# Performance work log

Measured on AMD Instinct MI355X. Metric: run time of the kernel, lower is better.

## Reference

```python
import jax, jax.numpy as jnp
import numpy as np

N_BUILDING = 30
N_SEMANTIC = 11
D_MODEL = 256
B_GRAPHS = 2048
EDGES_PER_GRAPH = 240
N_NODES = B_GRAPHS * N_BUILDING
N_EDGES = B_GRAPHS * EDGES_PER_GRAPH


def setup_inputs() -> dict:
    key = jax.random.key(0)
    ks = jax.random.split(key, 24)
    geometry = jax.random.normal(ks[0], (N_NODES, 5), dtype=jnp.float32)
    semantic = jax.random.randint(ks[1], (N_NODES,), 0, N_SEMANTIC)
    # within-graph edges
    src_l = jax.random.randint(ks[2], (N_EDGES,), 0, N_BUILDING)
    dst_l = jax.random.randint(ks[3], (N_EDGES,), 0, N_BUILDING)
    off = jnp.repeat(jnp.arange(B_GRAPHS) * N_BUILDING, EDGES_PER_GRAPH)
    edge_index = jnp.stack([src_l + off, dst_l + off])
    batch = jnp.repeat(jnp.arange(B_GRAPHS), N_BUILDING)

    def lin(k, i, o):
        k1, k2 = jax.random.split(k)
        s = 1.0 / np.sqrt(i)
        return (jax.random.uniform(k1, (i, o), jnp.float32, -s, s),
                jax.random.uniform(k2, (o,), jnp.float32, -s, s))

    W_geo, b_geo = lin(ks[4], 5, D_MODEL)
    emb = jax.random.normal(ks[5], (N_SEMANTIC, D_MODEL), dtype=jnp.float32)
    W_lot, b_lot = lin(ks[6], 2 * D_MODEL + N_BUILDING, D_MODEL)
    W_mp1, b_mp1 = lin(ks[7], 2 * D_MODEL, D_MODEL)
    W_mp2, b_mp2 = lin(ks[8], 2 * D_MODEL, D_MODEL)
    W_mp3, b_mp3 = lin(ks[9], 2 * D_MODEL, D_MODEL)
    W_agg, b_agg = lin(ks[10], 4 * D_MODEL, D_MODEL)
    W_mu, b_mu = lin(ks[11], D_MODEL, D_MODEL)
    W_var, b_var = lin(ks[12], D_MODEL, D_MODEL)
    return dict(geometry=geometry, semantic=semantic, edge_index=edge_index, batch=batch,
                W_geo=W_geo, b_geo=b_geo, emb=emb, W_lot=W_lot, b_lot=b_lot,
                W_mp1=W_mp1, b_mp1=b_mp1, W_mp2=W_mp2, b_mp2=b_mp2,
                W_mp3=W_mp3, b_mp3=b_mp3, W_agg=W_agg, b_agg=b_agg,
                W_mu=W_mu, b_mu=b_mu, W_var=W_var, b_var=b_var)


def _msgpass(x, src, dst, W, b):
    # PyG: x_i = x[dst] (target), x_j = x[src]; message = Linear(cat[x_i, x_j]); mean-aggregate at dst
    msgs = jnp.concatenate([x[dst], x[src]], axis=1) @ W + b  # [E, D]
    n = x.shape[0]
    s = jax.ops.segment_sum(msgs, dst, num_segments=n)
    cnt = jax.ops.segment_sum(jnp.ones((msgs.shape[0], 1), msgs.dtype), dst, num_segments=n)
    return s / jnp.maximum(cnt, 1.0)


def reference(geometry, semantic, edge_index, batch,
              W_geo, b_geo, emb, W_lot, b_lot,
              W_mp1, b_mp1, W_mp2, b_mp2, W_mp3, b_mp3,
              W_agg, b_agg, W_mu, b_mu, W_var, b_var):
    n_graphs = geometry.shape[0] // N_BUILDING
    src, dst = edge_index[0], edge_index[1]
    enc_geo = geometry @ W_geo + b_geo                       # [N, D]
    enc_sem = emb[semantic]                                   # [N, D]
    x_pos = jnp.tile(jnp.eye(N_BUILDING, dtype=jnp.float32), (n_graphs, 1))  # [N, 30]
    h = jnp.concatenate([enc_geo, enc_sem, x_pos], axis=1)
    h = jax.nn.relu(h @ W_lot + b_lot)
    g0 = jax.ops.segment_max(h, batch, num_segments=n_graphs)
    h = jax.nn.relu(_msgpass(h, src, dst, W_mp1, b_mp1))
    g1 = jax.ops.segment_max(h, batch, num_segments=n_graphs)
    h = jax.nn.relu(_msgpass(h, src, dst, W_mp2, b_mp2))
    g2 = jax.ops.segment_max(h, batch, num_segments=n_graphs)
    h = jax.nn.relu(_msgpass(h, src, dst, W_mp3, b_mp3))
    g3 = jax.ops.segment_max(h, batch, num_segments=n_graphs)
    g = jnp.concatenate([g0, g1, g2, g3], axis=1)             # [B, 4D]
    latent = g @ W_agg + b_agg
    mu = latent @ W_mu + b_mu
    log_var = latent @ W_var + b_var
    return mu, log_var
```

## Files before the change

kernel.cpp:

```cpp
#include <hip/hip_runtime.h>

typedef unsigned short u16;
typedef unsigned int u32;
typedef __attribute__((ext_vector_type(8))) short bf8;
typedef __attribute__((ext_vector_type(4))) float f4;
typedef __attribute__((ext_vector_type(4))) int i4;

#define NB  30
#define BG  2048
#define EPG 240
#define NEg (BG*EPG)
#define SA  260
#define SS  40
#define SL  264
#define SG  1032

#define WOFF_WT    0
#define WOFF_WAGG  786432
#define WOFF_WMU   (786432+524288)
#define WOFF_WVAR  (786432+524288+131072)
#define WOFF_TAB   (786432+524288+262144)
#define WOFF_G     (WOFF_TAB + 48128)
#define WOFF_FLAG  (WOFF_G + 4194304)

__device__ __forceinline__ float us2f(u16 u) {
    union { u32 i; float f; } v; v.i = ((u32)u) << 16; return v.f;
}
__device__ __forceinline__ u16 f2us(float f) {
    union { float f; u32 u; } v; v.f = f;
    u32 u = v.u;
    return (u16)((u + 0x7FFFu + ((u >> 16) & 1u)) >> 16);
}
__device__ __forceinline__ int ldidx(const void* p, long long i, int i64) {
    return i64 ? (int)((const long long*)p)[i] : ((const int*)p)[i];
}

__global__ __launch_bounds__(256) void prep_kernel(
    const float* __restrict__ Wmp1, const float* __restrict__ Wmp2,
    const float* __restrict__ Wmp3, const float* __restrict__ Wagg,
    const float* __restrict__ Wmu,  const float* __restrict__ Wvar,
    const float* __restrict__ W_geo, const float* __restrict__ b_geo,
    const float* __restrict__ emb,   const float* __restrict__ W_lot,
    const float* __restrict__ b_lot,
    const void* __restrict__ edge,  const void* __restrict__ semA,
    char* __restrict__ ws, int* __restrict__ flags)
{
    const int t = threadIdx.x;
    const int b = blockIdx.x;

    if (b == 209) {
        if (t == 0) {
            const int* e32 = (const int*)edge;
            int zc = 0;
            for (int j = 1; j <= 31; j += 2) if (e32[j] == 0) zc++;
            flags[0] = (zc == 16) ? 1 : 0;
            flags[1] = 0;
        }
        return;
    }

    if (b >= 192) {
        float* tab = (float*)(ws + WOFF_TAB);
        const int d = t, b2 = b - 192;
        if (b2 < 5) {
            float a = 0.f;
            #pragma unroll 8
            for (int k = 0; k < 256; ++k)
                a = fmaf(W_geo[b2*256 + k], W_lot[k*256 + d], a);
            tab[b2*256 + d] = a;
        } else if (b2 < 16) {
            const int s = b2 - 5;
            float a = 0.f;
            #pragma unroll 8
            for (int k = 0; k < 256; ++k)
                a = fmaf(emb[s*256 + k], W_lot[(256 + k)*256 + d], a);
            tab[1536 + s*256 + d] = a;
        } else {
            float a = b_lot[d];
            #pragma unroll 8
            for (int k = 0; k < 256; ++k)
                a = fmaf(b_geo[k], W_lot[k*256 + d], a);
            tab[1280 + d] = a;
            for (int p = 0; p < NB; ++p)
                tab[4352 + p*256 + d] = W_lot[(512 + p)*256 + d];
        }
        return;
    }

    __shared__ short tile[64 * 65];
    const float* W; u16* Wt; int K32, bk, bn;
    if (b < 96)       { const int r = b/32, tt = b%32;
                        W = (r==0)?Wmp1:((r==1)?Wmp2:Wmp3);
                        Wt = (u16*)(ws + WOFF_WT) + (size_t)r*256*512;
                        K32 = 16;  bk = tt/4;  bn = tt%4; }
    else if (b < 160) { const int tt = b-96;
                        W = Wagg; Wt = (u16*)(ws + WOFF_WAGG);
                        K32 = 32; bk = tt/4;  bn = tt%4; }
    else if (b < 176) { const int tt = b-160;
                        W = Wmu;  Wt = (u16*)(ws + WOFF_WMU);
                        K32 = 8;  bk = tt/4;  bn = tt%4; }
    else              { const int tt = b-176;
                        W = Wvar; Wt = (u16*)(ws + WOFF_WVAR);
                        K32 = 8;  bk = tt/4;  bn = tt%4; }

    const int r = t >> 6, c = t & 63;
    const int k0 = bk*64, n0 = bn*64;
    #pragma unroll
    for (int i = 0; i < 16; ++i) {
        const int kk = r + i*4;
        tile[kk*65 + c] = (short)f2us(W[(size_t)(k0 + kk)*256 + n0 + c]);
    }
    __syncthreads();

    const int lane = t >> 2;
    const int j0   = (t & 3) * 2;
    const int quad = lane >> 4, l16 = lane & 15;
    #pragma unroll
    for (int dk = 0; dk < 2; ++dk) {
        const int ktf = bk*2 + dk;
        #pragma unroll
        for (int nt = 0; nt < 4; ++nt) {
            const int chunk = (bn*K32 + ktf)*4 + nt;
            u32* dst = (u32*)(Wt + (size_t)chunk*512);
            const int kl = dk*32 + quad*8 + j0;
            const int nl = nt*16 + l16;
            const u32 v = (u32)(u16)tile[kl*65 + nl] |
                          ((u32)(u16)tile[(kl+1)*65 + nl] << 16);
            dst[t] = v;
        }
    }
}

__global__ __launch_bounds__(256, 4) void graph_kernel(
    const float* __restrict__ geometry,
    const void* __restrict__ semantic,
    const void* __restrict__ edge_index,
    const float* __restrict__ bmp1, const float* __restrict__ bmp2,
    const float* __restrict__ bmp3,
    const char* __restrict__ ws, u16* __restrict__ G,
    const int* __restrict__ flags)
{
    __shared__ __align__(16) short Ahi[32*SA];
    __shared__ __align__(16) short Shi[32*SS];
    __shared__ __align__(16) short Slo[32*SS];
    __shared__ int   cntN[32];
    __shared__ float geo_l[NB*5];
    __shared__ int   sem_l[NB];

    int* cntC = (int*)Ahi;

    const int tid  = threadIdx.x;
    const int g    = blockIdx.x;
    const int wave = tid >> 6, lane = tid & 63;
    const int l16  = lane & 15, quad = lane >> 4;

    const int i64 = flags[0];
    const u16* WtAll = (const u16*)(ws + WOFF_WT);
    const float* tab = (const float*)(ws + WOFF_TAB);

    {
        i4 z = {0, 0, 0, 0};
        ((i4*)cntC)[tid] = z;
        if (tid < 65) ((i4*)&Ahi[30*SA])[tid] = z;
        if (tid < 160) { ((i4*)Shi)[tid] = z; ((i4*)Slo)[tid] = z; }
        if (tid < 32) cntN[tid] = 0;
        if (tid < NB*5) geo_l[tid] = geometry[(size_t)g*NB*5 + tid];
        if (tid < NB)   sem_l[tid] = ldidx(semantic, g*NB + tid, i64);
    }
    __syncthreads();

    if (tid < EPG) {
        const long long e = (long long)g*EPG + tid;
        const int s  = ldidx(edge_index, e,                  i64) - g*NB;
        const int dd = ldidx(edge_index, (long long)NEg + e, i64) - g*NB;
        atomicAdd(&cntC[dd*32 + s], 1);
        atomicAdd(&cntN[dd], 1);
    }
    __syncthreads();

    for (int i = tid; i < 960; i += 256) {
        const int n = i >> 5, m = i & 31;
        const int c = cntC[n*32 + m], cn = cntN[n];
        const float v = (cn > 0) ? (float)c / (float)cn : 0.f;
        const u16 hi = f2us(v);
        Shi[n*SS + m] = (short)hi;
        Slo[n*SS + m] = (short)f2us(v - us2f(hi));
    }
    __syncthreads();

    {
        const int d = tid;
        const float m0 = tab[0*256+d], m1 = tab[1*256+d], m2 = tab[2*256+d],
                    m3 = tab[3*256+d], m4 = tab[4*256+d];
        const float cD = tab[1280 + d];
        float gmax = 0.f;
        for (int n = 0; n < NB; ++n) {
            const int s = sem_l[n];
            float a = cD + tab[1536 + s*256 + d] + tab[4352 + n*256 + d];
            a = fmaf(geo_l[n*5+0], m0, a); a = fmaf(geo_l[n*5+1], m1, a);
            a = fmaf(geo_l[n*5+2], m2, a); a = fmaf(geo_l[n*5+3], m3, a);
            a = fmaf(geo_l[n*5+4], m4, a);
            const float v = fmaxf(a, 0.f);
            Ahi[n*SA + d] = (short)f2us(v);
            gmax = fmaxf(gmax, v);
        }
        G[(size_t)g*1024 + d] = f2us(gmax);
    }
    __syncthreads();

    unsigned rmask = 0;
    #pragma unroll
    for (int mt = 0; mt < 2; ++mt)
        #pragma unroll
        for (int i = 0; i < 4; ++i) {
            const int row = mt*16 + quad*4 + i;
            if (row < NB && cntN[row] > 0) rmask |= 1u << (mt*4 + i);
        }

    bf8 sh[2], sl[2];
    #pragma unroll
    for (int mo = 0; mo < 2; ++mo) {
        sh[mo] = *(const bf8*)&Shi[(mo*16 + l16)*SS + quad*8];
        sl[mo] = *(const bf8*)&Slo[(mo*16 + l16)*SS + quad*8];
    }
    const int srcbase = ((quad & 1) << 5) | l16;
    const int mtsel   = quad >> 1;

    for (int r = 0; r < 3; ++r) {
        const u16* Wsw = WtAll + (size_t)r*131072;

        f4 C1[2][4], P[2][4];
        #pragma unroll
        for (int mt = 0; mt < 2; ++mt)
            #pragma unroll
            for (int nt = 0; nt < 4; ++nt) {
                C1[mt][nt] = (f4){0.f, 0.f, 0.f, 0.f};
                P [mt][nt] = (f4){0.f, 0.f, 0.f, 0.f};
            }

        #pragma unroll
        for (int kt = 0; kt < 8; ++kt) {
            bf8 ah[2];
            #pragma unroll
            for (int mt = 0; mt < 2; ++mt)
                ah[mt] = *(const bf8*)&Ahi[(mt*16 + l16)*SA + kt*32 + quad*8];
            #pragma unroll
            for (int nt = 0; nt < 4; ++nt) {
                const bf8 bt = *(const bf8*)&Wsw[(size_t)(((wave*16 + kt  )*4 + nt))*512 + lane*8];
                const bf8 bb = *(const bf8*)&Wsw[(size_t)(((wave*16 + kt+8)*4 + nt))*512 + lane*8];
                #pragma unroll
                for (int mt = 0; mt < 2; ++mt) {
                    C1[mt][nt] = __builtin_amdgcn_mfma_f32_16x16x32_bf16(ah[mt], bt, C1[mt][nt], 0, 0, 0);
                    P [mt][nt] = __builtin_amdgcn_mfma_f32_16x16x32_bf16(ah[mt], bb, P [mt][nt], 0, 0, 0);
                }
            }
        }

        unsigned pk[2][4][2];
        #pragma unroll
        for (int mt = 0; mt < 2; ++mt)
            #pragma unroll
            for (int nt = 0; nt < 4; ++nt) {
                pk[mt][nt][0] = (u32)f2us(P[mt][nt][0]) | ((u32)f2us(P[mt][nt][1]) << 16);
                pk[mt][nt][1] = (u32)f2us(P[mt][nt][2]) | ((u32)f2us(P[mt][nt][3]) << 16);
            }

        #pragma unroll
        for (int nt = 0; nt < 4; ++nt) {
            union { bf8 v; u32 u[4]; } bf_;
            #pragma unroll
            for (int t2 = 0; t2 < 4; ++t2) {
                const int src = srcbase + ((t2 >> 1) << 4);
                const u32 v0 = __shfl(pk[0][nt][t2 & 1], src, 64);
                const u32 v1 = __shfl(pk[1][nt][t2 & 1], src, 64);
                bf_.u[t2] = mtsel ? v1 : v0;
            }
            #pragma unroll
            for (int mo = 0; mo < 2; ++mo) {
                C1[mo][nt] = __builtin_amdgcn_mfma_f32_16x16x32_bf16(sh[mo], bf_.v, C1[mo][nt], 0, 0, 0);
                C1[mo][nt] = __builtin_amdgcn_mfma_f32_16x16x32_bf16(sl[mo], bf_.v, C1[mo][nt], 0, 0, 0);
            }
        }
        __syncthreads();

        const float* br = (r == 0) ? bmp1 : ((r == 1) ? bmp2 : bmp3);
        #pragma unroll
        for (int nt = 0; nt < 4; ++nt) {
            const int col = wave*64 + nt*16 + l16;
            const float bias = br[col];
            float cmax = 0.f;
            #pragma unroll
            for (int mt = 0; mt < 2; ++mt)
                #pragma unroll
                for (int i = 0; i < 4; ++i) {
                    const int row = mt*16 + quad*4 + i;
                    float v = fmaxf(C1[mt][nt][i] + bias, 0.f);
                    if (!((rmask >> (mt*4 + i)) & 1u)) v = 0.f;
                    Ahi[row*SA + col] = (short)f2us(v);
                    cmax = fmaxf(cmax, v);
                }
            cmax = fmaxf(cmax, __shfl_xor(cmax, 16, 64));
            cmax = fmaxf(cmax, __shfl_xor(cmax, 32, 64));
            if (quad == 0)
                G[(size_t)g*1024 + (r+1)*256 + col] = f2us(cmax);
        }
        __syncthreads();
    }
}

__global__ __launch_bounds__(256, 4) void head_kernel(
    const char* __restrict__ ws, const u16* __restrict__ G,
    const float* __restrict__ bagg, const float* __restrict__ bmu,
    const float* __restrict__ bvar, float* __restrict__ out)
{
    __shared__ __align__(16) short Gs[8*SG];
    __shared__ __align__(16) short Lhi[16*SL];
    __shared__ __align__(16) short Llo[16*SL];

    const int tid  = threadIdx.x;
    const int wave = tid >> 6, lane = tid & 63;
    const int l16  = lane & 15, quad = lane >> 4;
    const int g0   = blockIdx.x * 8;

    const u16* WtA = (const u16*)(ws + WOFF_WAGG);
    const u16* WtM = (const u16*)(ws + WOFF_WMU);
    const u16* WtV = (const u16*)(ws + WOFF_WVAR);

    #pragma unroll
    for (int rr = 0; rr < 8; ++rr) {
        ((u32*)&Gs[rr*SG])[tid]       = ((const u32*)&G[(size_t)(g0+rr)*1024])[tid];
        ((u32*)&Gs[rr*SG])[tid + 256] = ((const u32*)&G[(size_t)(g0+rr)*1024])[tid + 256];
    }
    __syncthreads();

    f4 acc[4];
    #pragma unroll
    for (int nt = 0; nt < 4; ++nt) acc[nt] = (f4){0.f, 0.f, 0.f, 0.f};

    #pragma unroll 8
    for (int kt = 0; kt < 32; ++kt) {
        const bf8 ah = *(const bf8*)&Gs[(l16 & 7)*SG + kt*32 + quad*8];
        #pragma unroll
        for (int nt = 0; nt < 4; ++nt) {
            const bf8 b = *(const bf8*)&WtA[(size_t)((wave*32 + kt)*4 + nt)*512 + lane*8];
            acc[nt] = __builtin_amdgcn_mfma_f32_16x16x32_bf16(ah, b, acc[nt], 0, 0, 0);
        }
    }
    #pragma unroll
    for (int nt = 0; nt < 4; ++nt) {
        const int col = wave*64 + nt*16 + l16;
        const float bias = bagg[col];
        #pragma unroll
        for (int i = 0; i < 4; ++i) {
            const int row = quad*4 + i;
            const float v = acc[nt][i] + bias;
            const u16 hi = f2us(v);
            Lhi[row*SL + col] = (short)hi;
            Llo[row*SL + col] = (short)f2us(v - us2f(hi));
        }
    }
    __syncthreads();

    f4 am[4], av[4];
    #pragma unroll
    for (int nt = 0; nt < 4; ++nt) {
        am[nt] = (f4){0.f, 0.f, 0.f, 0.f};
        av[nt] = (f4){0.f, 0.f, 0.f, 0.f};
    }
    #pragma unroll
    for (int kt = 0; kt < 8; ++kt) {
        const bf8 ah = *(const bf8*)&Lhi[l16*SL + kt*32 + quad*8];
        const bf8 al = *(const bf8*)&Llo[l16*SL + kt*32 + quad*8];
        #pragma unroll
        for (int nt = 0; nt < 4; ++nt) {
            const bf8 bm_ = *(const bf8*)&WtM[(size_t)((wave*8 + kt)*4 + nt)*512 + lane*8];
            const bf8 bv_ = *(const bf8*)&WtV[(size_t)((wave*8 + kt)*4 + nt)*512 + lane*8];
            am[nt] = __builtin_amdgcn_mfma_f32_16x16x32_bf16(ah, bm_, am[nt], 0, 0, 0);
            am[nt] = __builtin_amdgcn_mfma_f32_16x16x32_bf16(al, bm_, am[nt], 0, 0, 0);
            av[nt] = __builtin_amdgcn_mfma_f32_16x16x32_bf16(ah, bv_, av[nt], 0, 0, 0);
            av[nt] = __builtin_amdgcn_mfma_f32_16x16x32_bf16(al, bv_, av[nt], 0, 0, 0);
        }
    }
    #pragma unroll
    for (int nt = 0; nt < 4; ++nt) {
        const int col = wave*64 + nt*16 + l16;
        const float b1 = bmu[col], b2 = bvar[col];
        #pragma unroll
        for (int i = 0; i < 4; ++i) {
            const int r = quad*4 + i;
            if (r < 8) {
                const int row = g0 + r;
                out[(size_t)row*256 + col]          = am[nt][i] + b1;
                out[524288 + (size_t)row*256 + col] = av[nt][i] + b2;
            }
        }
    }
}

extern "C" void kernel_launch(void* const* d_in, const int* in_sizes, int n_in,
                              void* d_out, int out_size, void* d_ws, size_t ws_size,
                              hipStream_t stream)
{
    const float* geometry  = (const float*)d_in[0];
    const void*  semantic  = d_in[1];
    const void*  edge_ix   = d_in[2];
    const float* W_geo = (const float*)d_in[4];
    const float* b_geo = (const float*)d_in[5];
    const float* emb   = (const float*)d_in[6];
    const float* W_lot = (const float*)d_in[7];
    const float* b_lot = (const float*)d_in[8];
    const float* Wmp1  = (const float*)d_in[9];
    const float* bmp1  = (const float*)d_in[10];
    const float* Wmp2  = (const float*)d_in[11];
    const float* bmp2  = (const float*)d_in[12];
    const float* Wmp3  = (const float*)d_in[13];
    const float* bmp3  = (const float*)d_in[14];
    const float* Wagg  = (const float*)d_in[15];
    const float* bagg  = (const float*)d_in[16];
    const float* Wmu   = (const float*)d_in[17];
    const float* bmu   = (const float*)d_in[18];
    const float* Wvar  = (const float*)d_in[19];
    const float* bvar  = (const float*)d_in[20];

    char* ws    = (char*)d_ws;
    int*  flags = (int*)(ws + WOFF_FLAG);
    u16*  G     = (u16*)(ws + WOFF_G);

    prep_kernel<<<210, 256, 0, stream>>>(Wmp1, Wmp2, Wmp3, Wagg, Wmu, Wvar,
                                         W_geo, b_geo, emb, W_lot, b_lot,
                                         edge_ix, semantic, ws, flags);
    graph_kernel<<<BG, 256, 0, stream>>>(geometry, semantic, edge_ix,
                                         bmp1, bmp2, bmp3, ws, G, flags);
    head_kernel<<<256, 256, 0, stream>>>(ws, G, bagg, bmu, bvar, (float*)d_out);
}
```

Measured before the change: 237.2 us.

## Process two graphs per block in graph_kernel to reuse weight fragments

Each block of graph_kernel now handles two graphs, holding two sets of LDS buffers and accumulators, so every weight fragment loaded from global memory feeds MFMAs for both graphs. The aim is to halve the weight traffic per graph in the three message-passing rounds. In exchange the block doubles its LDS use and accumulator registers, launch bounds drop from 4 to 3 waves per SIMD, and only 1024 blocks are launched, which may reduce occupancy and latency hiding.

After: 341.0 us. 43.8% more time.

```diff
diff --git a/kernel.cpp b/kernel.cpp
--- a/kernel.cpp
+++ b/kernel.cpp
@@ -131,7 +131,7 @@
     }
 }
 
-__global__ __launch_bounds__(256, 4) void graph_kernel(
+__global__ __launch_bounds__(256, 3) void graph_kernel(
     const float* __restrict__ geometry,
     const void* __restrict__ semantic,
     const void* __restrict__ edge_index,
@@ -140,17 +140,15 @@
     const char* __restrict__ ws, u16* __restrict__ G,
     const int* __restrict__ flags)
 {
-    __shared__ __align__(16) short Ahi[32*SA];
-    __shared__ __align__(16) short Shi[32*SS];
-    __shared__ __align__(16) short Slo[32*SS];
-    __shared__ int   cntN[32];
-    __shared__ float geo_l[NB*5];
-    __shared__ int   sem_l[NB];
-
-    int* cntC = (int*)Ahi;
+    __shared__ __align__(16) short Ahi[2][32*SA];
+    __shared__ __align__(16) short Shi[2][32*SS];
+    __shared__ __align__(16) short Slo[2][32*SS];
+    __shared__ int   cntN[2][32];
+    __shared__ float geo_l[2][NB*5];
+    __shared__ int   sem_l[2][NB];
 
     const int tid  = threadIdx.x;
-    const int g    = blockIdx.x;
+    const int g0   = blockIdx.x * 2;
     const int wave = tid >> 6, lane = tid & 63;
     const int l16  = lane & 15, quad = lane >> 4;
 
@@ -160,31 +158,42 @@
 
     {
         i4 z = {0, 0, 0, 0};
-        ((i4*)cntC)[tid] = z;
-        if (tid < 65) ((i4*)&Ahi[30*SA])[tid] = z;
-        if (tid < 160) { ((i4*)Shi)[tid] = z; ((i4*)Slo)[tid] = z; }
-        if (tid < 32) cntN[tid] = 0;
-        if (tid < NB*5) geo_l[tid] = geometry[(size_t)g*NB*5 + tid];
-        if (tid < NB)   sem_l[tid] = ldidx(semantic, g*NB + tid, i64);
+        #pragma unroll
+        for (int gg = 0; gg < 2; ++gg) {
+            ((i4*)&Ahi[gg][0])[tid] = z;
+            if (tid < 65) ((i4*)&Ahi[gg][30*SA])[tid] = z;
+            if (tid < 160) { ((i4*)&Shi[gg][0])[tid] = z; ((i4*)&Slo[gg][0])[tid] = z; }
+            if (tid < 32) cntN[gg][tid] = 0;
+            if (tid < NB*5) geo_l[gg][tid] = geometry[(size_t)(g0+gg)*NB*5 + tid];
+            if (tid < NB)   sem_l[gg][tid] = ldidx(semantic, (g0+gg)*NB + tid, i64);
+        }
     }
     __syncthreads();
 
     if (tid < EPG) {
-        const long long e = (long long)g*EPG + tid;
-        const int s  = ldidx(edge_index, e,                  i64) - g*NB;
-        const int dd = ldidx(edge_index, (long long)NEg + e, i64) - g*NB;
-        atomicAdd(&cntC[dd*32 + s], 1);
-        atomicAdd(&cntN[dd], 1);
-    }
-    __syncthreads();
-
-    for (int i = tid; i < 960; i += 256) {
-        const int n = i >> 5, m = i & 31;
-        const int c = cntC[n*32 + m], cn = cntN[n];
-        const float v = (cn > 0) ? (float)c / (float)cn : 0.f;
-        const u16 hi = f2us(v);
-        Shi[n*SS + m] = (short)hi;
-        Slo[n*SS + m] = (short)f2us(v - us2f(hi));
+        #pragma unroll
+        for (int gg = 0; gg < 2; ++gg) {
+            int* cntC = (int*)&Ahi[gg][0];
+            const long long e = (long long)(g0+gg)*EPG + tid;
+            const int s  = ldidx(edge_index, e,                  i64) - (g0+gg)*NB;
+            const int dd = ldidx(edge_index, (long long)NEg + e, i64) - (g0+gg)*NB;
+            atomicAdd(&cntC[dd*32 + s], 1);
+            atomicAdd(&cntN[gg][dd], 1);
+        }
+    }
+    __syncthreads();
+
+    #pragma unroll
+    for (int gg = 0; gg < 2; ++gg) {
+        const int* cntC = (const int*)&Ahi[gg][0];
+        for (int i = tid; i < 960; i += 256) {
+            const int n = i >> 5, m = i & 31;
+            const int c = cntC[n*32 + m], cn = cntN[gg][n];
+            const float v = (cn > 0) ? (float)c / (float)cn : 0.f;
+            const u16 hi = f2us(v);
+            Shi[gg][n*SS + m] = (short)hi;
+            Slo[gg][n*SS + m] = (short)f2us(v - us2f(hi));
+        }
     }
     __syncthreads();
 
@@ -193,92 +202,107 @@
         const float m0 = tab[0*256+d], m1 = tab[1*256+d], m2 = tab[2*256+d],
                     m3 = tab[3*256+d], m4 = tab[4*256+d];
         const float cD = tab[1280 + d];
-        float gmax = 0.f;
-        for (int n = 0; n < NB; ++n) {
-            const int s = sem_l[n];
-            float a = cD + tab[1536 + s*256 + d] + tab[4352 + n*256 + d];
-            a = fmaf(geo_l[n*5+0], m0, a); a = fmaf(geo_l[n*5+1], m1, a);
-            a = fmaf(geo_l[n*5+2], m2, a); a = fmaf(geo_l[n*5+3], m3, a);
-            a = fmaf(geo_l[n*5+4], m4, a);
-            const float v = fmaxf(a, 0.f);
-            Ahi[n*SA + d] = (short)f2us(v);
-            gmax = fmaxf(gmax, v);
-        }
-        G[(size_t)g*1024 + d] = f2us(gmax);
-    }
-    __syncthreads();
-
-    unsigned rmask = 0;
-    #pragma unroll
-    for (int mt = 0; mt < 2; ++mt)
-        #pragma unroll
-        for (int i = 0; i < 4; ++i) {
-            const int row = mt*16 + quad*4 + i;
-            if (row < NB && cntN[row] > 0) rmask |= 1u << (mt*4 + i);
-        }
-
-    bf8 sh[2], sl[2];
-    #pragma unroll
-    for (int mo = 0; mo < 2; ++mo) {
-        sh[mo] = *(const bf8*)&Shi[(mo*16 + l16)*SS + quad*8];
-        sl[mo] = *(const bf8*)&Slo[(mo*16 + l16)*SS + quad*8];
-    }
+        #pragma unroll
+        for (int gg = 0; gg < 2; ++gg) {
+            float gmax = 0.f;
+            for (int n = 0; n < NB; ++n) {
+                const int s = sem_l[gg][n];
+                float a = cD + tab[1536 + s*256 + d] + tab[4352 + n*256 + d];
+                a = fmaf(geo_l[gg][n*5+0], m0, a); a = fmaf(geo_l[gg][n*5+1], m1, a);
+                a = fmaf(geo_l[gg][n*5+2], m2, a); a = fmaf(geo_l[gg][n*5+3], m3, a);
+                a = fmaf(geo_l[gg][n*5+4], m4, a);
+                const float v = fmaxf(a, 0.f);
+                Ahi[gg][n*SA + d] = (short)f2us(v);
+                gmax = fmaxf(gmax, v);
+            }
+            G[(size_t)(g0+gg)*1024 + d] = f2us(gmax);
+        }
+    }
+    __syncthreads();
+
+    unsigned rmask[2] = {0, 0};
+    #pragma unroll
+    for (int gg = 0; gg < 2; ++gg)
+        #pragma unroll
+        for (int mt = 0; mt < 2; ++mt)
+            #pragma unroll
+            for (int i = 0; i < 4; ++i) {
+                const int row = mt*16 + quad*4 + i;
+                if (row < NB && cntN[gg][row] > 0) rmask[gg] |= 1u << (mt*4 + i);
+            }
+
+    bf8 sh[2][2], sl[2][2];
+    #pragma unroll
+    for (int gg = 0; gg < 2; ++gg)
+        #pragma unroll
+        for (int mo = 0; mo < 2; ++mo) {
+            sh[gg][mo] = *(const bf8*)&Shi[gg][(mo*16 + l16)*SS + quad*8];
+            sl[gg][mo] = *(const bf8*)&Slo[gg][(mo*16 + l16)*SS + quad*8];
+        }
     const int srcbase = ((quad & 1) << 5) | l16;
     const int mtsel   = quad >> 1;
 
     for (int r = 0; r < 3; ++r) {
         const u16* Wsw = WtAll + (size_t)r*131072;
 
-        f4 C1[2][4], P[2][4];
-        #pragma unroll
-        for (int mt = 0; mt < 2; ++mt)
-            #pragma unroll
-            for (int nt = 0; nt < 4; ++nt) {
-                C1[mt][nt] = (f4){0.f, 0.f, 0.f, 0.f};
-                P [mt][nt] = (f4){0.f, 0.f, 0.f, 0.f};
-            }
+        f4 C1[2][2][4], P[2][2][4];
+        #pragma unroll
+        for (int gg = 0; gg < 2; ++gg)
+            #pragma unroll
+            for (int mt = 0; mt < 2; ++mt)
+                #pragma unroll
+                for (int nt = 0; nt < 4; ++nt) {
+                    C1[gg][mt][nt] = (f4){0.f, 0.f, 0.f, 0.f};
+                    P [gg][mt][nt] = (f4){0.f, 0.f, 0.f, 0.f};
+                }
 
         #pragma unroll
         for (int kt = 0; kt < 8; ++kt) {
-            bf8 ah[2];
-            #pragma unroll
-            for (int mt = 0; mt < 2; ++mt)
-                ah[mt] = *(const bf8*)&Ahi[(mt*16 + l16)*SA + kt*32 + quad*8];
+            bf8 ah[2][2];
+            #pragma unroll
+            for (int gg = 0; gg < 2; ++gg)
+                #pragma unroll
+                for (int mt = 0; mt < 2; ++mt)
+                    ah[gg][mt] = *(const bf8*)&Ahi[gg][(mt*16 + l16)*SA + kt*32 + quad*8];
             #pragma unroll
             for (int nt = 0; nt < 4; ++nt) {
                 const bf8 bt = *(const bf8*)&Wsw[(size_t)(((wave*16 + kt  )*4 + nt))*512 + lane*8];
                 const bf8 bb = *(const bf8*)&Wsw[(size_t)(((wave*16 + kt+8)*4 + nt))*512 + lane*8];
                 #pragma unroll
-                for (int mt = 0; mt < 2; ++mt) {
-                    C1[mt][nt] = __builtin_amdgcn_mfma_f32_16x16x32_bf16(ah[mt], bt, C1[mt][nt], 0, 0, 0);
-                    P [mt][nt] = __builtin_amdgcn_mfma_f32_16x16x32_bf16(ah[mt], bb, P [mt][nt], 0, 0, 0);
+                for (int gg = 0; gg < 2; ++gg)
+                    #pragma unroll
+                    for (int mt = 0; mt < 2; ++mt) {
+                        C1[gg][mt][nt] = __builtin_amdgcn_mfma_f32_16x16x32_bf16(ah[gg][mt], bt, C1[gg][mt][nt], 0, 0, 0);
+                        P [gg][mt][nt] = __builtin_amdgcn_mfma_f32_16x16x32_bf16(ah[gg][mt], bb, P [gg][mt][nt], 0, 0, 0);
+                    }
+            }
+        }
+
+        #pragma unroll
+        for (int gg = 0; gg < 2; ++gg) {
+            unsigned pk[2][4][2];
+            #pragma unroll
+            for (int mt = 0; mt < 2; ++mt)
+                #pragma unroll
+                for (int nt = 0; nt < 4; ++nt) {
+                    pk[mt][nt][0] = (u32)f2us(P[gg][mt][nt][0]) | ((u32)f2us(P[gg][mt][nt][1]) << 16);
+                    pk[mt][nt][1] = (u32)f2us(P[gg][mt][nt][2]) | ((u32)f2us(P[gg][mt][nt][3]) << 16);
                 }
-            }
-        }
-
-        unsigned pk[2][4][2];
-        #pragma unroll
-        for (int mt = 0; mt < 2; ++mt)
             #pragma unroll
             for (int nt = 0; nt < 4; ++nt) {
-                pk[mt][nt][0] = (u32)f2us(P[mt][nt][0]) | ((u32)f2us(P[mt][nt][1]) << 16);
-                pk[mt][nt][1] = (u32)f2us(P[mt][nt][2]) | ((u32)f2us(P[mt][nt][3]) << 16);
-            }
-
-        #pragma unroll
-        for (int nt = 0; nt < 4; ++nt) {
-            union { bf8 v; u32 u[4]; } bf_;
-            #pragma unroll
-            for (int t2 = 0; t2 < 4; ++t2) {
-                const int src = srcbase + ((t2 >> 1) << 4);
-                const u32 v0 = __shfl(pk[0][nt][t2 & 1], src, 64);
-                const u32 v1 = __shfl(pk[1][nt][t2 & 1], src, 64);
-                bf_.u[t2] = mtsel ? v1 : v0;
-            }
-            #pragma unroll
-            for (int mo = 0; mo < 2; ++mo) {
-                C1[mo][nt] = __builtin_amdgcn_mfma_f32_16x16x32_bf16(sh[mo], bf_.v, C1[mo][nt], 0, 0, 0);
-                C1[mo][nt] = __builtin_amdgcn_mfma_f32_16x16x32_bf16(sl[mo], bf_.v, C1[mo][nt], 0, 0, 0);
+                union { bf8 v; u32 u[4]; } bf_;
+                #pragma unroll
+                for (int t2 = 0; t2 < 4; ++t2) {
+                    const int src = srcbase + ((t2 >> 1) << 4);
+                    const u32 v0 = __shfl(pk[0][nt][t2 & 1], src, 64);
+                    const u32 v1 = __shfl(pk[1][nt][t2 & 1], src, 64);
+                    bf_.u[t2] = mtsel ? v1 : v0;
+                }
+                #pragma unroll
+                for (int mo = 0; mo < 2; ++mo) {
+                    C1[gg][mo][nt] = __builtin_amdgcn_mfma_f32_16x16x32_bf16(sh[gg][mo], bf_.v, C1[gg][mo][nt], 0, 0, 0);
+                    C1[gg][mo][nt] = __builtin_amdgcn_mfma_f32_16x16x32_bf16(sl[gg][mo], bf_.v, C1[gg][mo][nt], 0, 0, 0);
+                }
             }
         }
         __syncthreads();
@@ -288,21 +312,24 @@
         for (int nt = 0; nt < 4; ++nt) {
             const int col = wave*64 + nt*16 + l16;
             const float bias = br[col];
-            float cmax = 0.f;
-            #pragma unroll
-            for (int mt = 0; mt < 2; ++mt)
-                #pragma unroll
-                for (int i = 0; i < 4; ++i) {
-                    const int row = mt*16 + quad*4 + i;
-                    float v = fmaxf(C1[mt][nt][i] + bias, 0.f);
-                    if (!((rmask >> (mt*4 + i)) & 1u)) v = 0.f;
-                    Ahi[row*SA + col] = (short)f2us(v);
-                    cmax = fmaxf(cmax, v);
-                }
-            cmax = fmaxf(cmax, __shfl_xor(cmax, 16, 64));
-            cmax = fmaxf(cmax, __shfl_xor(cmax, 32, 64));
-            if (quad == 0)
-                G[(size_t)g*1024 + (r+1)*256 + col] = f2us(cmax);
+            #pragma unroll
+            for (int gg = 0; gg < 2; ++gg) {
+                float cmax = 0.f;
+                #pragma unroll
+                for (int mt = 0; mt < 2; ++mt)
+                    #pragma unroll
+                    for (int i = 0; i < 4; ++i) {
+                        const int row = mt*16 + quad*4 + i;
+                        float v = fmaxf(C1[gg][mt][nt][i] + bias, 0.f);
+                        if (!((rmask[gg] >> (mt*4 + i)) & 1u)) v = 0.f;
+                        Ahi[gg][row*SA + col] = (short)f2us(v);
+                        cmax = fmaxf(cmax, v);
+                    }
+                cmax = fmaxf(cmax, __shfl_xor(cmax, 16, 64));
+                cmax = fmaxf(cmax, __shfl_xor(cmax, 32, 64));
+                if (quad == 0)
+                    G[(size_t)(g0+gg)*1024 + (r+1)*256 + col] = f2us(cmax);
+            }
         }
         __syncthreads();
     }
@@ -429,7 +456,7 @@
     prep_kernel<<<210, 256, 0, stream>>>(Wmp1, Wmp2, Wmp3, Wagg, Wmu, Wvar,
                                          W_geo, b_geo, emb, W_lot, b_lot,
                                          edge_ix, semantic, ws, flags);
-    graph_kernel<<<BG, 256, 0, stream>>>(geometry, semantic, edge_ix,
-                                         bmp1, bmp2, bmp3, ws, G, flags);
+    graph_kernel<<<BG/2, 256, 0, stream>>>(geometry, semantic, edge_ix,
+                                           bmp1, bmp2, bmp3, ws, G, flags);
     head_kernel<<<256, 256, 0, stream>>>(ws, G, bagg, bmu, bvar, (float*)d_out);
 }
```
